# Kernel optimization log

Measured on AMD Instinct MI355X. Metric: run time of the kernel, lower is better.

Reference implementation:

```python
import jax, jax.numpy as jnp
import numpy as np

N = 2_000_000          # number of neurons in this layer
M = 2_000_000          # total rows across prior layers (concatenated source)
U = 1024               # number of unique (deduplicated) weight matrices
R, C = 8, 8            # per-neuron weight matrix shape [out_dim, in_dim]


def setup_inputs() -> dict:
    key = jax.random.key(0)
    k1, k2, k3, k4 = jax.random.split(key, 4)
    values = jax.random.normal(k1, (M, C), dtype=jnp.float32)      # concatenated layer_values
    weights = jax.random.normal(k2, (U, R, C), dtype=jnp.float32)  # deduplicated weight store
    input_idx = jax.random.randint(k3, (N,), 0, M, dtype=jnp.int32)   # multi-layer gather map
    weight_idx = jax.random.randint(k4, (N,), 0, U, dtype=jnp.int32)  # weight gather map
    return {"values": values, "weights": weights,
            "input_idx": input_idx, "weight_idx": weight_idx}


def reference(values, weights, input_idx, weight_idx):
    # self.gather(layer_values): irregular gather of input rows -> [N, C]
    x = jnp.take(values, input_idx, axis=0)
    # self.gather_weights(w): gather per-neuron weight matrices -> [N, R, C]
    w = jnp.take(weights, weight_idx, axis=0)
    # y = w @ input_values : per-neuron small matmul -> [N, R]
    y = jnp.einsum("nrc,nc->nr", w, x)
    return y
```

## Files before the change

kernel.cpp:

```cpp
#include <hip/hip_runtime.h>


typedef float f32x4 __attribute__((ext_vector_type(4)));
typedef unsigned int u32;
typedef u32 u32x4 __attribute__((ext_vector_type(4)));
typedef __fp16 f16x2 __attribute__((ext_vector_type(2)));

#define NPT   2
#define BLOCK 1024
#define U_MATS 1024

union HU { u32 u; f16x2 h; };

__global__ __launch_bounds__(BLOCK) void neuron_gemv_kernel(
    const f32x4* __restrict__ values,
    const f32x4* __restrict__ weights,
    const int*   __restrict__ input_idx,
    const int*   __restrict__ weight_idx,
    f32x4*       __restrict__ out,
    int N, int T)
{
    __shared__ u32 wlds[U_MATS * 32];

    for (int g = threadIdx.x; g < U_MATS * 16; g += BLOCK) {
        f32x4 v = weights[g];
        int u = g >> 4;
        int e = g & 15;
        int r = e >> 1;
        int h = e & 1;
        int dst = u * 32 + (((r + u) & 7) << 2) + h * 2;
        HU a, b;
        a.h = f16x2{(__fp16)v.x, (__fp16)v.y};
        b.h = f16x2{(__fp16)v.z, (__fp16)v.w};
        wlds[dst + 0] = a.u;
        wlds[dst + 1] = b.u;
    }
    __syncthreads();

    const u32x4* wl4 = (const u32x4*)wlds;

    int tid = blockIdx.x * BLOCK + threadIdx.x;

    int  n[NPT];
    bool act[NPT];
#pragma unroll
    for (int k = 0; k < NPT; ++k) {
        n[k]   = tid + k * T;
        act[k] = n[k] < N;
    }

    int ii[NPT], wi[NPT];
#pragma unroll
    for (int k = 0; k < NPT; ++k) {
        ii[k] = act[k] ? input_idx[n[k]]  : 0;
        wi[k] = act[k] ? weight_idx[n[k]] : 0;
    }

    f32x4 x0[NPT], x1[NPT];
#pragma unroll
    for (int k = 0; k < NPT; ++k) {
        x0[k] = values[(size_t)ii[k] * 2 + 0];
        x1[k] = values[(size_t)ii[k] * 2 + 1];
    }

#pragma unroll
    for (int k = 0; k < NPT; ++k) {
        if (!act[k]) continue;
        int base = wi[k] * 8;
        int rot  = wi[k] & 7;
        float y[8];
#pragma unroll
        for (int r = 0; r < 8; ++r) {
            u32x4 wr = wl4[base + ((r + rot) & 7)];
            HU p0, p1, p2, p3;
            p0.u = wr.x; p1.u = wr.y; p2.u = wr.z; p3.u = wr.w;
            y[r] = (float)p0.h.x * x0[k].x + (float)p0.h.y * x0[k].y
                 + (float)p1.h.x * x0[k].z + (float)p1.h.y * x0[k].w
                 + (float)p2.h.x * x1[k].x + (float)p2.h.y * x1[k].y
                 + (float)p3.h.x * x1[k].z + (float)p3.h.y * x1[k].w;
        }
        f32x4 o0 = { y[0], y[1], y[2], y[3] };
        f32x4 o1 = { y[4], y[5], y[6], y[7] };
        out[(size_t)n[k] * 2 + 0] = o0;
        out[(size_t)n[k] * 2 + 1] = o1;
    }
}

extern "C" void kernel_launch(void* const* d_in, const int* in_sizes, int n_in,
                              void* d_out, int out_size, void* d_ws, size_t ws_size,
                              hipStream_t stream) {
    const f32x4* values  = (const f32x4*)d_in[0];
    const f32x4* weights = (const f32x4*)d_in[1];
    const int*   iidx    = (const int*)d_in[2];
    const int*   widx    = (const int*)d_in[3];
    f32x4*       out     = (f32x4*)d_out;

    int N = in_sizes[2];

    const int grid = (N + BLOCK * NPT - 1) / (BLOCK * NPT);
    const int T    = grid * BLOCK;
    neuron_gemv_kernel<<<grid, BLOCK, 0, stream>>>(values, weights, iidx, widx, out, N, T);
}
```

Baseline: 73.28 us.

## Use persistent grid with software-prefetched indices to amortize LDS weight staging

Replaces the one-shot grid with a fixed grid of 256 persistent blocks that loop over neurons, four per thread per iteration. The fp16 weight table is staged into LDS once per block instead of once per ~2048 neurons, and the next iteration's index loads are issued before the current compute. This reduces redundant weight staging traffic and overlaps index fetches with gathers, at the cost of more registers and fixed parallelism tied to the grid size.

```diff
diff --git a/kernel.cpp b/kernel.cpp
--- a/kernel.cpp
+++ b/kernel.cpp
@@ -6,8 +6,9 @@
 typedef u32 u32x4 __attribute__((ext_vector_type(4)));
 typedef __fp16 f16x2 __attribute__((ext_vector_type(2)));
 
-#define NPT   2
-#define BLOCK 1024
+#define NPT    4
+#define BLOCK  1024
+#define GRID   256
 #define U_MATS 1024
 
 union HU { u32 u; f16x2 h; };
@@ -18,7 +19,7 @@
     const int*   __restrict__ input_idx,
     const int*   __restrict__ weight_idx,
     f32x4*       __restrict__ out,
-    int N, int T)
+    int N)
 {
     __shared__ u32 wlds[U_MATS * 32];
 
@@ -39,50 +40,66 @@
 
     const u32x4* wl4 = (const u32x4*)wlds;
 
-    int tid = blockIdx.x * BLOCK + threadIdx.x;
+    const int  T   = GRID * BLOCK;
+    const int  tid = blockIdx.x * BLOCK + threadIdx.x;
 
-    int  n[NPT];
-    bool act[NPT];
+    int ii[NPT], wi[NPT], iin[NPT], win[NPT];
+
+    long base = tid;
 #pragma unroll
-    for (int k = 0; k < NPT; ++k) {
-        n[k]   = tid + k * T;
-        act[k] = n[k] < N;
+    for (int j = 0; j < NPT; ++j) {
+        long n  = base + (long)j * T;
+        int  nc = (n < N) ? (int)n : 0;
+        ii[j] = input_idx[nc];
+        wi[j] = weight_idx[nc];
     }
 
-    int ii[NPT], wi[NPT];
+    while (base < N) {
+        long nextbase = base + (long)T * NPT;
+
+        f32x4 x0[NPT], x1[NPT];
 #pragma unroll
-    for (int k = 0; k < NPT; ++k) {
-        ii[k] = act[k] ? input_idx[n[k]]  : 0;
-        wi[k] = act[k] ? weight_idx[n[k]] : 0;
-    }
+        for (int j = 0; j < NPT; ++j) {
+            x0[j] = values[(size_t)ii[j] * 2 + 0];
+            x1[j] = values[(size_t)ii[j] * 2 + 1];
+        }
 
-    f32x4 x0[NPT], x1[NPT];
+        if (nextbase < N) {
 #pragma unroll
-    for (int k = 0; k < NPT; ++k) {
-        x0[k] = values[(size_t)ii[k] * 2 + 0];
-        x1[k] = values[(size_t)ii[k] * 2 + 1];
-    }
+            for (int j = 0; j < NPT; ++j) {
+                long n  = nextbase + (long)j * T;
+                int  nc = (n < N) ? (int)n : 0;
+                iin[j] = input_idx[nc];
+                win[j] = weight_idx[nc];
+            }
+        }
 
 #pragma unroll
-    for (int k = 0; k < NPT; ++k) {
-        if (!act[k]) continue;
-        int base = wi[k] * 8;
-        int rot  = wi[k] & 7;
-        float y[8];
+        for (int j = 0; j < NPT; ++j) {
+            long n = base + (long)j * T;
+            if (n >= N) continue;
+            int b   = wi[j] * 8;
+            int rot = wi[j] & 7;
+            float y[8];
 #pragma unroll
-        for (int r = 0; r < 8; ++r) {
-            u32x4 wr = wl4[base + ((r + rot) & 7)];
-            HU p0, p1, p2, p3;
-            p0.u = wr.x; p1.u = wr.y; p2.u = wr.z; p3.u = wr.w;
-            y[r] = (float)p0.h.x * x0[k].x + (float)p0.h.y * x0[k].y
-                 + (float)p1.h.x * x0[k].z + (float)p1.h.y * x0[k].w
-                 + (float)p2.h.x * x1[k].x + (float)p2.h.y * x1[k].y
-                 + (float)p3.h.x * x1[k].z + (float)p3.h.y * x1[k].w;
+            for (int r = 0; r < 8; ++r) {
+                u32x4 wr = wl4[b + ((r + rot) & 7)];
+                HU p0, p1, p2, p3;
+                p0.u = wr.x; p1.u = wr.y; p2.u = wr.z; p3.u = wr.w;
+                y[r] = (float)p0.h.x * x0[j].x + (float)p0.h.y * x0[j].y
+                     + (float)p1.h.x * x0[j].z + (float)p1.h.y * x0[j].w
+                     + (float)p2.h.x * x1[j].x + (float)p2.h.y * x1[j].y
+                     + (float)p3.h.x * x1[j].z + (float)p3.h.y * x1[j].w;
+            }
+            f32x4 o0 = { y[0], y[1], y[2], y[3] };
+            f32x4 o1 = { y[4], y[5], y[6], y[7] };
+            out[(size_t)n * 2 + 0] = o0;
+            out[(size_t)n * 2 + 1] = o1;
         }
-        f32x4 o0 = { y[0], y[1], y[2], y[3] };
-        f32x4 o1 = { y[4], y[5], y[6], y[7] };
-        out[(size_t)n[k] * 2 + 0] = o0;
-        out[(size_t)n[k] * 2 + 1] = o1;
+
+        base = nextbase;
+#pragma unroll
+        for (int j = 0; j < NPT; ++j) { ii[j] = iin[j]; wi[j] = win[j]; }
     }
 }
 
@@ -97,7 +114,5 @@
 
     int N = in_sizes[2];
 
-    const int grid = (N + BLOCK * NPT - 1) / (BLOCK * NPT);
-    const int T    = grid * BLOCK;
-    neuron_gemv_kernel<<<grid, BLOCK, 0, stream>>>(values, weights, iidx, widx, out, N, T);
+    neuron_gemv_kernel<<<GRID, BLOCK, 0, stream>>>(values, weights, iidx, widx, out, N);
 }
```

Result: faster. 59.05 us (median of 2 runs) (-19.4%).
